# Kernel tuning notes

Hardware: AMD Instinct MI355X
Metric: run time of the kernel (lower is better)

## Reference

```python
import jax, jax.numpy as jnp
import numpy as np

B = 128          # batch size
N_KG = 500       # KG vertices
N = N_KG + 2     # + sensor node + zero target node
D = 1024         # embed_dim (hard-coded in forward)
H = 256          # gnn_hidden
E = 4000         # edges
EPS = 1e-5


def setup_inputs() -> dict:
    key = jax.random.key(0)
    ks = jax.random.split(key, 8)
    return {
        "sensor_batch": jax.random.normal(ks[0], (B, D), jnp.float32),
        "base_vertices": jax.random.normal(ks[1], (N_KG, D), jnp.float32),
        "edge_index": jax.random.randint(ks[2], (2, E), 0, N, jnp.int64),
        "W1": jax.random.normal(ks[3], (D, H), jnp.float32) * (1.0 / np.sqrt(D)),
        "b1": jnp.zeros((H,), jnp.float32),
        "gamma1": jnp.ones((H,), jnp.float32),
        "beta1": jnp.zeros((H,), jnp.float32),
        "W2": jax.random.normal(ks[4], (H, H), jnp.float32) * (1.0 / np.sqrt(H)),
        "b2": jnp.zeros((H,), jnp.float32),
        "gamma2": jnp.ones((H,), jnp.float32),
        "beta2": jnp.zeros((H,), jnp.float32),
        "W3": jax.random.normal(ks[5], (H, H), jnp.float32) * (1.0 / np.sqrt(H)),
        "b3": jnp.zeros((H,), jnp.float32),
        "gamma3": jnp.ones((H,), jnp.float32),
        "beta3": jnp.zeros((H,), jnp.float32),
    }


def _gcn_norm(edge_index):
    # add self loops, symmetric normalization D^{-1/2} A D^{-1/2}
    loops = jnp.arange(N, dtype=edge_index.dtype)
    src = jnp.concatenate([edge_index[0], loops])
    dst = jnp.concatenate([edge_index[1], loops])
    deg = jnp.zeros((N,), jnp.float32).at[dst].add(1.0)
    dinv = jnp.where(deg > 0, jax.lax.rsqrt(deg), 0.0)
    norm = dinv[src] * dinv[dst]   # [E+N]
    return src, dst, norm


def _gcn_conv(x, W, b, src, dst, norm):
    # x: [B, N, F_in] -> [B, N, F_out]
    h = jnp.einsum('bnf,fh->bnh', x, W)
    msg = h[:, src, :] * norm[None, :, None]            # gather + scale
    out = jnp.zeros_like(h).at[:, dst, :].add(msg)      # scatter-add
    return out + b


def _bn_elu(x, gamma, beta):
    # BatchNorm1d over flattened (B*N, H) in training mode, then ELU
    Bn, Nn, Hh = x.shape
    xf = x.reshape(Bn * Nn, Hh)
    mean = jnp.mean(xf, axis=0)
    var = jnp.mean(jnp.square(xf - mean), axis=0)  # biased, as in torch BN fwd
    y = (xf - mean) * jax.lax.rsqrt(var + EPS) * gamma + beta
    return jax.nn.elu(y).reshape(Bn, Nn, Hh)


def reference(sensor_batch, base_vertices, edge_index,
              W1, b1, gamma1, beta1,
              W2, b2, gamma2, beta2,
              W3, b3, gamma3, beta3):
    Bn = sensor_batch.shape[0]
    # x = [base_vertices; sensor_input; zeros] per batch element -> [B, N, D]
    base = jnp.broadcast_to(base_vertices[None], (Bn, N_KG, D))
    zeros = jnp.zeros((Bn, 1, D), sensor_batch.dtype)
    x = jnp.concatenate([base, sensor_batch[:, None, :], zeros], axis=1)

    src, dst, norm = _gcn_norm(edge_index)
    x = _bn_elu(_gcn_conv(x, W1, b1, src, dst, norm), gamma1, beta1)
    x = _bn_elu(_gcn_conv(x, W2, b2, src, dst, norm), gamma2, beta2)
    x = _bn_elu(_gcn_conv(x, W3, b3, src, dst, norm), gamma3, beta3)
    return x
```

## Files before the change

kernel.cpp:

```cpp
#include <hip/hip_runtime.h>
#include <cstdint>
#include <cstddef>

#define NNODES 502
#define NKG    500
#define NPAD   512
#define NEDGE  4000
#define NET    4502
#define BB     128
#define DD     1024
#define HH     256
#define MROWS  (BB*NNODES)
#define MT     65536
#define MCAT   628
#define EPITCH 136

typedef short short8 __attribute__((ext_vector_type(8)));
typedef float f32x4  __attribute__((ext_vector_type(4)));

__device__ __forceinline__ unsigned short f2bf(float f) {
  union { float f; unsigned int u; } v; v.f = f;
  unsigned int r = v.u + 0x7fffu + ((v.u >> 16) & 1u);
  return (unsigned short)(r >> 16);
}

__device__ __forceinline__ float bf2f(unsigned short u) {
  union { unsigned int u; float f; } v; v.u = ((unsigned int)u) << 16;
  return v.f;
}

__device__ __forceinline__ float elu(float y) {
  return (y > 0.f) ? y : (__expf(y) - 1.f);
}

__device__ __forceinline__ void stage16(const void* g, void* l) {
  __builtin_amdgcn_global_load_lds((__attribute__((address_space(1))) void*)g,
                                   (__attribute__((address_space(3))) void*)l, 16, 0, 0);
}

__device__ __forceinline__ void mfma16(f32x4& c, short8 a, short8 b) {
  asm volatile("v_mfma_f32_16x16x32_bf16 %0, %1, %2, %0" : "+v"(c) : "v"(a), "v"(b));
}

__device__ inline void get_edge(const int* __restrict__ e, int i, int i64mode,
                                int& src, int& dst) {
  if (i < NEDGE) {
    if (i64mode) { src = e[2*i]; dst = e[2*NEDGE + 2*i]; }
    else         { src = e[i];   dst = e[NEDGE + i]; }
  } else {
    src = dst = i - NEDGE;
  }
  src = min(max(src, 0), NNODES-1);
  dst = min(max(dst, 0), NNODES-1);
}

__global__ void detect_kernel(const int* __restrict__ e, int* __restrict__ flag) {
  int v = e[2*threadIdx.x + 1];
  if (v != 0) atomicOr(flag, 1);
}

__global__ void deg_kernel(const int* __restrict__ e, const int* __restrict__ flag,
                           int* __restrict__ deg) {
  int i = blockIdx.x*256 + threadIdx.x;
  if (i >= NET) return;
  int src, dst; get_edge(e, i, *flag == 0, src, dst);
  atomicAdd(&deg[dst], 1);
}

__global__ void scan_kernel(const int* __restrict__ deg, float* __restrict__ dinv,
                            int* __restrict__ rp, int* __restrict__ cursor) {
  __shared__ int s[512];
  int t = threadIdx.x;
  int cnt = (t < NNODES) ? deg[t] : 0;
  s[t] = cnt;
  if (t < NNODES) dinv[t] = rsqrtf((float)cnt);
  __syncthreads();
  for (int off = 1; off < 512; off <<= 1) {
    int v = (t >= off) ? s[t-off] : 0;
    __syncthreads();
    s[t] += v;
    __syncthreads();
  }
  if (t == 0) rp[0] = 0;
  if (t < NNODES) { rp[t+1] = s[t]; cursor[t] = s[t] - cnt; }
}

__global__ void fill_kernel(const int* __restrict__ e, const int* __restrict__ flag,
                            const float* __restrict__ dinv, int* __restrict__ cursor,
                            int* __restrict__ colA, float* __restrict__ valA) {
  int i = blockIdx.x*256 + threadIdx.x;
  if (i >= NET) return;
  int src, dst; get_edge(e, i, *flag == 0, src, dst);
  int pos = atomicAdd(&cursor[dst], 1);
  colA[pos] = src;
  valA[pos] = dinv[src] * dinv[dst];
}

__global__ void sdf_kernel(const int* __restrict__ e, const int* __restrict__ flag,
                           const float* __restrict__ dinv, float* __restrict__ Sdf) {
  int i = blockIdx.x*256 + threadIdx.x;
  if (i >= NET) return;
  int src, dst; get_edge(e, i, *flag == 0, src, dst);
  atomicAdd(&Sdf[dst*NPAD + src], dinv[src]*dinv[dst]);
}

__global__ void sdcvt_kernel(const float* __restrict__ Sdf, unsigned short* __restrict__ Sd) {
  int i = blockIdx.x*256 + threadIdx.x;
  Sd[i] = f2bf(Sdf[i]);
}

__global__ __launch_bounds__(256) void prep_kernel(
    const float* __restrict__ W1, const float* __restrict__ W2, const float* __restrict__ W3,
    const float* __restrict__ base, const float* __restrict__ sensor,
    unsigned short* __restrict__ Wt1, unsigned short* __restrict__ Wt2,
    unsigned short* __restrict__ Wt3, unsigned short* __restrict__ Xp1) {
  int bid = blockIdx.x, tid = threadIdx.x;
  if (bid < 512) {
    const float* W = (bid & 256) ? W3 : W2;
    unsigned short* Wt = (bid & 256) ? Wt3 : Wt2;
    int n = bid & 255;
    Wt[n*HH + tid] = f2bf(W[(size_t)tid*HH + n]);
  } else if (bid < 768) {
    int n = bid - 512;
    for (int k = tid; k < DD; k += 256)
      Wt1[n*DD + k] = f2bf(W1[(size_t)k*HH + n]);
  } else {
    int i = (bid - 768)*256 + tid;
    int r = i >> 8, c = (i & 255) * 4;
    float4 v = make_float4(0.f, 0.f, 0.f, 0.f);
    if (r < NKG) v = *(const float4*)&base[(size_t)r*DD + c];
    else if (r < MCAT) v = *(const float4*)&sensor[(size_t)(r-NKG)*DD + c];
    union { unsigned short u[4]; uint2 d; } p;
    p.u[0]=f2bf(v.x); p.u[1]=f2bf(v.y); p.u[2]=f2bf(v.z); p.u[3]=f2bf(v.w);
    *(uint2*)&Xp1[(size_t)r*DD + c] = p.d;
  }
}

__global__ __launch_bounds__(256) void gemm1m_kernel(
    const unsigned short* __restrict__ Ag,
    const unsigned short* __restrict__ Bg,
    float* __restrict__ C) {
  __shared__ unsigned short As[128*32];
  __shared__ unsigned short Bs[128*32];
  int tid = threadIdx.x;
  int wave = tid >> 6, lane = tid & 63;
  int l15 = lane & 15, quad = lane >> 4;
  int wm = (wave & 1) * 64, wn = (wave >> 1) * 64;
  int row0 = blockIdx.y * 128, col0 = blockIdx.x * 128;
  f32x4 acc[4][4] = {};
  for (int k0 = 0; k0 < DD; k0 += 32) {
#pragma unroll
    for (int q = 0; q < 2; ++q) {
      int c = wave*128 + q*64 + lane;
      stage16(Ag + (size_t)(row0 + (c>>2))*DD + k0 + (c&3)*8, As + c*8);
      stage16(Bg + (size_t)(col0 + (c>>2))*DD + k0 + (c&3)*8, Bs + c*8);
    }
    __syncthreads();
    short8 af[4], bfv[4];
#pragma unroll
    for (int i = 0; i < 4; ++i) {
      af[i]  = *(const short8*)(As + (wm + i*16 + l15)*32 + quad*8);
      bfv[i] = *(const short8*)(Bs + (wn + i*16 + l15)*32 + quad*8);
    }
#pragma unroll
    for (int mi = 0; mi < 4; ++mi)
#pragma unroll
      for (int ni = 0; ni < 4; ++ni)
        mfma16(acc[mi][ni], af[mi], bfv[ni]);
    __syncthreads();
  }
  asm volatile("s_nop 7\n\ts_nop 7" ::);
#pragma unroll
  for (int ni = 0; ni < 4; ++ni) {
    int n = col0 + wn + ni*16 + l15;
#pragma unroll
    for (int mi = 0; mi < 4; ++mi) {
      int m = row0 + wm + mi*16 + quad*4;
#pragma unroll
      for (int r = 0; r < 4; ++r)
        if (m + r < MCAT) C[(size_t)(m+r)*HH + n] = acc[mi][ni][r];
    }
  }
}

__global__ void ac_kernel(const int* __restrict__ rp, const int* __restrict__ colA,
                          const float* __restrict__ valA, const float* __restrict__ hcat,
                          float* __restrict__ Abuf, float* __restrict__ cbuf) {
  int n = blockIdx.x, h = threadIdx.x;
  int s = rp[n], e = rp[n+1];
  float acc = 0.f, cacc = 0.f;
  for (int t = s; t < e; ++t) {
    int cl = colA[t]; float v = valA[t];
    if (cl < NKG) acc += v * hcat[cl*HH + h];
    else if (cl == NKG) cacc += v;
  }
  Abuf[n*HH + h] = acc;
  if (h == 0) cbuf[n] = cacc;
}

__global__ __launch_bounds__(256) void bn1n_kernel(
    const float* __restrict__ Abuf, const float* __restrict__ cbuf,
    const float* __restrict__ hcat,
    float* __restrict__ sA1, float* __restrict__ sAA1, float* __restrict__ sAc1,
    float* __restrict__ scp, float* __restrict__ ssA, float* __restrict__ sssA) {
  int bid = blockIdx.x, h = threadIdx.x;
  if (bid < 32) {
    int n0 = bid*16, n1 = min(n0+16, NNODES);
    float sA = 0, sAA = 0, sAc = 0, sc = 0, scc = 0;
    for (int n = n0; n < n1; ++n) {
      float a = Abuf[n*HH + h]; float cn = cbuf[n];
      sA += a; sAA += a*a; sAc += a*cn; sc += cn; scc += cn*cn;
    }
    atomicAdd(&sA1[h], sA); atomicAdd(&sAA1[h], sAA); atomicAdd(&sAc1[h], sAc);
    if (h == 0) { atomicAdd(&scp[0], sc); atomicAdd(&scp[1], scc); }
  } else {
    int b0 = (bid-32)*16;
    float ss = 0, sss = 0;
    for (int b = b0; b < b0+16; ++b) {
      float v = hcat[(size_t)(NKG + b)*HH + h]; ss += v; sss += v*v;
    }
    atomicAdd(&ssA[h], ss); atomicAdd(&sssA[h], sss);
  }
}

__global__ void fin1_kernel(const float* __restrict__ sA1, const float* __restrict__ sAA1,
                            const float* __restrict__ sAc1, const float* __restrict__ scp,
                            const float* __restrict__ ssA, const float* __restrict__ sssA,
                            const float* __restrict__ gamma, const float* __restrict__ beta,
                            float* __restrict__ scale, float* __restrict__ shift) {
  int h = threadIdx.x;
  float sA = sA1[h], sAA = sAA1[h], sAc = sAc1[h];
  float sc = scp[0], scc = scp[1];
  float ss = ssA[h], sss = sssA[h];
  const float cnt = (float)MROWS;
  float mean = ((float)BB * sA + sc*ss) / cnt;
  float msq  = ((float)BB * sAA + 2.f*sAc*ss + scc*sss) / cnt;
  float var  = msq - mean*mean;
  float scl  = gamma[h] * rsqrtf(var + 1e-5f);
  scale[h] = scl; shift[h] = beta[h] - mean*scl;
}

__global__ __launch_bounds__(256) void x2_kernel(
    const float* __restrict__ Abuf, const float* __restrict__ cbuf,
    const float* __restrict__ hcat, const float* __restrict__ scale,
    const float* __restrict__ shift, unsigned short* __restrict__ Xb) {
  int idx = blockIdx.x*256 + threadIdx.x;
  int row = idx >> 6, h0 = (idx & 63)*4;
  int b = row >> 9, n = row & (NPAD-1);
  union { unsigned short u[4]; uint2 d; } p;
  p.d = make_uint2(0,0);
  if (n < NNODES) {
    float4 a  = *(const float4*)(Abuf + n*HH + h0);
    float4 s  = *(const float4*)(hcat + (size_t)(NKG + b)*HH + h0);
    float4 sc = *(const float4*)(scale + h0);
    float4 sh = *(const float4*)(shift + h0);
    float cn = cbuf[n];
    p.u[0] = f2bf(elu((a.x + cn*s.x)*sc.x + sh.x));
    p.u[1] = f2bf(elu((a.y + cn*s.y)*sc.y + sh.y));
    p.u[2] = f2bf(elu((a.z + cn*s.z)*sc.z + sh.z));
    p.u[3] = f2bf(elu((a.w + cn*s.w)*sc.w + sh.w));
  }
  *(uint2*)(Xb + (size_t)row*HH + h0) = p.d;
}

__global__ __launch_bounds__(256) void gemmT_kernel(
    const unsigned short* __restrict__ Ag,
    const unsigned short* __restrict__ Bg,
    unsigned short* __restrict__ Tt) {
  __shared__ __align__(16) unsigned short smem[128*EPITCH];
  unsigned short* As = smem;
  unsigned short* Bs = smem + 8192;
  int tid = threadIdx.x;
  int wave = tid >> 6, lane = tid & 63;
  int l15 = lane & 15, quad = lane >> 4;
  int wm = (wave & 1) * 64, wn = (wave >> 1) * 64;
  int row0 = blockIdx.y * 128, col0 = blockIdx.x * 128;
  f32x4 acc[4][4] = {};
  for (int k0 = 0; k0 < HH; k0 += 64) {
#pragma unroll
    for (int q = 0; q < 4; ++q) {
      int c = q*256 + wave*64 + lane;
      int half = c >> 9, rr = (c >> 2) & 127, j = c & 3;
      stage16(Ag + (size_t)(row0 + rr)*HH + k0 + half*32 + j*8, As + c*8);
      stage16(Bg + (size_t)(col0 + rr)*HH + k0 + half*32 + j*8, Bs + c*8);
    }
    __syncthreads();
#pragma unroll
    for (int kb = 0; kb < 2; ++kb) {
      short8 af[4], bfv[4];
#pragma unroll
      for (int i = 0; i < 4; ++i) {
        af[i]  = *(const short8*)(As + kb*4096 + (wm + i*16 + l15)*32 + quad*8);
        bfv[i] = *(const short8*)(Bs + kb*4096 + (wn + i*16 + l15)*32 + quad*8);
      }
#pragma unroll
      for (int mi = 0; mi < 4; ++mi)
#pragma unroll
        for (int ni = 0; ni < 4; ++ni)
          mfma16(acc[mi][ni], af[mi], bfv[ni]);
    }
    __syncthreads();
  }
  asm volatile("s_nop 7\n\ts_nop 7" ::);
#pragma unroll
  for (int ni = 0; ni < 4; ++ni) {
    int nl = wn + ni*16 + l15;
#pragma unroll
    for (int mi = 0; mi < 4; ++mi) {
      int ml = wm + mi*16 + quad*4;
#pragma unroll
      for (int r = 0; r < 4; ++r)
        smem[nl*EPITCH + ml + r] = f2bf(acc[mi][ni][r]);
    }
  }
  __syncthreads();
  int moff = (tid & 15)*8;
#pragma unroll
  for (int j = 0; j < 8; ++j) {
    int nr = (tid >> 4) + j*16;
    uint4 d = *(const uint4*)(smem + nr*EPITCH + moff);
    *(uint4*)(Tt + (size_t)(col0 + nr)*MT + row0 + moff) = d;
  }
}

__global__ __launch_bounds__(256) void gemmS_kernel(
    const unsigned short* __restrict__ Sd,
    const unsigned short* __restrict__ Tt,
    unsigned short* __restrict__ Xbo,
    float* __restrict__ sums, float* __restrict__ ssqs) {
  __shared__ __align__(16) unsigned short smem[128*EPITCH];
  unsigned short* As = smem;
  unsigned short* Bs = smem + 8192;
  int tid = threadIdx.x;
  int wave = tid >> 6, lane = tid & 63;
  int l15 = lane & 15, quad = lane >> 4;
  int wm = (wave & 1) * 64, wn = (wave >> 1) * 64;
  int id = blockIdx.x;
  int xcd = id & 7;
  int w = id >> 3;
  int y = w & 3;
  int g = (w >> 2) * 8 + xcd;
  int x = g >> 7;
  int b = g & 127;
  int row0 = y * 128, col0 = x * 128;
  f32x4 acc[4][4] = {};
  for (int k0 = 0; k0 < NPAD; k0 += 64) {
#pragma unroll
    for (int q = 0; q < 4; ++q) {
      int c = q*256 + wave*64 + lane;
      int half = c >> 9, rr = (c >> 2) & 127, j = c & 3;
      stage16(Sd + (size_t)(row0 + rr)*NPAD + k0 + half*32 + j*8, As + c*8);
      stage16(Tt + (size_t)(col0 + rr)*MT + b*NPAD + k0 + half*32 + j*8, Bs + c*8);
    }
    __syncthreads();
#pragma unroll
    for (int kb = 0; kb < 2; ++kb) {
      short8 af[4], bfv[4];
#pragma unroll
      for (int i = 0; i < 4; ++i) {
        af[i]  = *(const short8*)(As + kb*4096 + (wm + i*16 + l15)*32 + quad*8);
        bfv[i] = *(const short8*)(Bs + kb*4096 + (wn + i*16 + l15)*32 + quad*8);
      }
#pragma unroll
      for (int mi = 0; mi < 4; ++mi)
#pragma unroll
        for (int ni = 0; ni < 4; ++ni)
          mfma16(acc[mi][ni], af[mi], bfv[ni]);
    }
    __syncthreads();
  }
  asm volatile("s_nop 7\n\ts_nop 7" ::);
  float ps[4] = {0,0,0,0}, pq[4] = {0,0,0,0};
#pragma unroll
  for (int ni = 0; ni < 4; ++ni)
#pragma unroll
    for (int mi = 0; mi < 4; ++mi)
#pragma unroll
      for (int r = 0; r < 4; ++r) {
        float v = acc[mi][ni][r];
        ps[ni] += v; pq[ni] += v*v;
      }
#pragma unroll
  for (int mi = 0; mi < 4; ++mi) {
    int ml = wm + mi*16 + quad*4;
#pragma unroll
    for (int ni = 0; ni < 4; ++ni) {
      int nl = wn + ni*16 + l15;
#pragma unroll
      for (int r = 0; r < 4; ++r)
        smem[(ml + r)*EPITCH + nl] = f2bf(acc[mi][ni][r]);
    }
  }
  __syncthreads();
  unsigned short* Xrow = Xbo + (size_t)b*NPAD*HH;
  int noff = (tid & 15)*8;
#pragma unroll
  for (int j = 0; j < 8; ++j) {
    int rr = (tid >> 4) + j*16;
    int node = row0 + rr;
    if (node < NNODES) {
      uint4 d = *(const uint4*)(smem + rr*EPITCH + noff);
      *(uint4*)(Xrow + (size_t)node*HH + col0 + noff) = d;
    }
  }
  __syncthreads();
  float* red = (float*)smem;
  red[tid] = 0.f;
  __syncthreads();
#pragma unroll
  for (int ni = 0; ni < 4; ++ni) {
    int cl = wn + ni*16 + l15;
    atomicAdd(&red[cl], ps[ni]);
    atomicAdd(&red[128+cl], pq[ni]);
  }
  __syncthreads();
  if (tid < 128) atomicAdd(&sums[col0+tid], red[tid]);
  else atomicAdd(&ssqs[col0+tid-128], red[tid]);
}

__global__ void finalize_kernel(const float* __restrict__ sums, const float* __restrict__ ssqs,
                                const float* __restrict__ gamma, const float* __restrict__ beta,
                                float* __restrict__ scale, float* __restrict__ shift) {
  int h = threadIdx.x;
  const float cnt = (float)MROWS;
  float mean = sums[h] / cnt;
  float var  = ssqs[h] / cnt - mean*mean;
  float scl  = gamma[h] * rsqrtf(var + 1e-5f);
  scale[h] = scl; shift[h] = beta[h] - mean*scl;
}

__global__ __launch_bounds__(256) void bnip_kernel(
    unsigned short* __restrict__ Xb, const float* __restrict__ scale,
    const float* __restrict__ shift) {
  int idx = blockIdx.x*256 + threadIdx.x;
  int row = idx >> 6, h0 = (idx & 63)*4;
  int n = row & (NPAD-1);
  if (n >= NNODES) return;
  unsigned short* p = Xb + (size_t)row*HH + h0;
  union { unsigned short u[4]; uint2 d; } v;
  v.d = *(uint2*)p;
  float4 sc = *(const float4*)(scale + h0);
  float4 sh = *(const float4*)(shift + h0);
  v.u[0] = f2bf(elu(bf2f(v.u[0])*sc.x + sh.x));
  v.u[1] = f2bf(elu(bf2f(v.u[1])*sc.y + sh.y));
  v.u[2] = f2bf(elu(bf2f(v.u[2])*sc.z + sh.z));
  v.u[3] = f2bf(elu(bf2f(v.u[3])*sc.w + sh.w));
  *(uint2*)p = v.d;
}

__global__ __launch_bounds__(256) void bnout_kernel(
    const unsigned short* __restrict__ Xb, const float* __restrict__ scale,
    const float* __restrict__ shift, float* __restrict__ O) {
  int idx = blockIdx.x*256 + threadIdx.x;
  int row = idx >> 6, h0 = (idx & 63)*4;
  int b = row >> 9, n = row & (NPAD-1);
  if (n >= NNODES) return;
  union { unsigned short u[4]; uint2 d; } v;
  v.d = *(const uint2*)(Xb + (size_t)row*HH + h0);
  float4 sc = *(const float4*)(scale + h0);
  float4 sh = *(const float4*)(shift + h0);
  float4 o;
  o.x = elu(bf2f(v.u[0])*sc.x + sh.x);
  o.y = elu(bf2f(v.u[1])*sc.y + sh.y);
  o.z = elu(bf2f(v.u[2])*sc.z + sh.z);
  o.w = elu(bf2f(v.u[3])*sc.w + sh.w);
  *(float4*)(O + ((size_t)(b*NNODES + n)*HH + h0)) = o;
}

extern "C" void kernel_launch(void* const* d_in, const int* in_sizes, int n_in,
                              void* d_out, int out_size, void* d_ws, size_t ws_size,
                              hipStream_t stream) {
  const float* sensor = (const float*)d_in[0];
  const float* base   = (const float*)d_in[1];
  const int*   eidx   = (const int*)d_in[2];
  const float* W1 = (const float*)d_in[3];
  const float* g1 = (const float*)d_in[5];
  const float* be1= (const float*)d_in[6];
  const float* W2 = (const float*)d_in[7];
  const float* g2 = (const float*)d_in[9];
  const float* be2= (const float*)d_in[10];
  const float* W3 = (const float*)d_in[11];
  const float* g3 = (const float*)d_in[13];
  const float* be3= (const float*)d_in[14];

  char* ws = (char*)d_ws;
  int*   deg    = (int*)(ws + 0);
  float* sum2   = (float*)(ws + 2048);
  float* ssq2   = (float*)(ws + 3072);
  float* sum3   = (float*)(ws + 4096);
  float* ssq3   = (float*)(ws + 5120);
  float* cbuf   = (float*)(ws + 6144);
  int*   cursor = (int*)(ws + 8192);
  int*   flag   = (int*)(ws + 10240);
  float* sA1    = (float*)(ws + 10496);
  float* sAA1   = (float*)(ws + 11520);
  float* sAc1   = (float*)(ws + 12544);
  float* scp    = (float*)(ws + 13568);
  float* ssA    = (float*)(ws + 13824);
  float* sssA   = (float*)(ws + 14848);
  float* dinv   = (float*)(ws + 16384);
  int*   rp     = (int*)(ws + 18432);
  int*   colA   = (int*)(ws + 20480);
  float* valA   = (float*)(ws + 40960);
  float* scale1 = (float*)(ws + 61440);
  float* shift1 = (float*)(ws + 62464);
  float* scale2 = (float*)(ws + 63488);
  float* shift2 = (float*)(ws + 64512);
  float* scale3 = (float*)(ws + 65536);
  float* shift3 = (float*)(ws + 66560);
  float* Abuf   = (float*)(ws + 67584);
  float* hcat   = (float*)(ws + 581632);
  unsigned short* Wt2 = (unsigned short*)(ws + 1224704);
  unsigned short* Wt3 = (unsigned short*)(ws + 1355776);
  unsigned short* Sd  = (unsigned short*)(ws + 1486848);
  unsigned short* Xb  = (unsigned short*)(ws + 2011136);
  unsigned short* Tt  = (unsigned short*)(ws + 35565568UL);
  unsigned short* Xp1 = (unsigned short*)(ws + 35565568UL);
  unsigned short* Wt1 = (unsigned short*)(ws + 35565568UL + 1310720);
  float* out = (float*)d_out;
  float* Sdf = (float*)d_out;

  hipMemsetAsync(ws, 0, 16384, stream);
  hipMemsetAsync(d_out, 0, NPAD*NPAD*4, stream);
  detect_kernel<<<1, 256, 0, stream>>>(eidx, flag);
  deg_kernel<<<(NET+255)/256, 256, 0, stream>>>(eidx, flag, deg);
  scan_kernel<<<1, 512, 0, stream>>>(deg, dinv, rp, cursor);
  fill_kernel<<<(NET+255)/256, 256, 0, stream>>>(eidx, flag, dinv, cursor, colA, valA);
  sdf_kernel<<<(NET+255)/256, 256, 0, stream>>>(eidx, flag, dinv, Sdf);
  sdcvt_kernel<<<(NPAD*NPAD)/256, 256, 0, stream>>>(Sdf, Sd);
  prep_kernel<<<1408, 256, 0, stream>>>(W1, W2, W3, base, sensor, Wt1, Wt2, Wt3, Xp1);

  gemm1m_kernel<<<dim3(2, 5), 256, 0, stream>>>(Xp1, Wt1, hcat);
  ac_kernel<<<NNODES, 256, 0, stream>>>(rp, colA, valA, hcat, Abuf, cbuf);
  bn1n_kernel<<<40, 256, 0, stream>>>(Abuf, cbuf, hcat, sA1, sAA1, sAc1, scp, ssA, sssA);
  fin1_kernel<<<1, 256, 0, stream>>>(sA1, sAA1, sAc1, scp, ssA, sssA, g1, be1, scale1, shift1);
  x2_kernel<<<(MT*64)/256, 256, 0, stream>>>(Abuf, cbuf, hcat, scale1, shift1, Xb);

  gemmT_kernel<<<dim3(2, MT/128), 256, 0, stream>>>(Xb, Wt2, Tt);
  gemmS_kernel<<<1024, 256, 0, stream>>>(Sd, Tt, Xb, sum2, ssq2);
  finalize_kernel<<<1, 256, 0, stream>>>(sum2, ssq2, g2, be2, scale2, shift2);
  bnip_kernel<<<(MT*64)/256, 256, 0, stream>>>(Xb, scale2, shift2);

  gemmT_kernel<<<dim3(2, MT/128), 256, 0, stream>>>(Xb, Wt3, Tt);
  gemmS_kernel<<<1024, 256, 0, stream>>>(Sd, Tt, Xb, sum3, ssq3);
  finalize_kernel<<<1, 256, 0, stream>>>(sum3, ssq3, g3, be3, scale3, shift3);
  bnout_kernel<<<(MT*64)/256, 256, 0, stream>>>(Xb, scale3, shift3, out);
}
```

Measured before the change: 323.7 us.

## Fuse BN2+ELU into layer-3 GEMM prologue, split-K first GEMM, merge graph prep kernels

The layer-2 batch-norm finalize and in-place BN/ELU pass are folded into the prologue of the layer-3 transform GEMM. Each block computes scale and shift from the sums and applies BN+ELU to its A tile while staging it. The transform GEMM now covers all 256 output columns per block, so A is read once instead of twice, at the cost of more accumulator registers. The first GEMM is split four ways along K with atomicAdd into a zeroed output to expose more blocks. Edge-format detection, the fill step and the Sdf scatter are merged into fewer kernels to cut launch overhead.

```diff
diff --git a/kernel.cpp b/kernel.cpp
--- a/kernel.cpp
+++ b/kernel.cpp
@@ -54,16 +54,20 @@
   dst = min(max(dst, 0), NNODES-1);
 }
 
-__global__ void detect_kernel(const int* __restrict__ e, int* __restrict__ flag) {
-  int v = e[2*threadIdx.x + 1];
-  if (v != 0) atomicOr(flag, 1);
-}
-
-__global__ void deg_kernel(const int* __restrict__ e, const int* __restrict__ flag,
-                           int* __restrict__ deg) {
+__device__ __forceinline__ int detect_mode(const int* __restrict__ e) {
+  __shared__ int sflag;
+  if (threadIdx.x == 0) sflag = 0;
+  __syncthreads();
+  if (e[2*threadIdx.x + 1] != 0) atomicOr(&sflag, 1);
+  __syncthreads();
+  return sflag == 0;
+}
+
+__global__ void deg_kernel(const int* __restrict__ e, int* __restrict__ deg) {
+  int i64 = detect_mode(e);
   int i = blockIdx.x*256 + threadIdx.x;
   if (i >= NET) return;
-  int src, dst; get_edge(e, i, *flag == 0, src, dst);
+  int src, dst; get_edge(e, i, i64, src, dst);
   atomicAdd(&deg[dst], 1);
 }
 
@@ -85,23 +89,18 @@
   if (t < NNODES) { rp[t+1] = s[t]; cursor[t] = s[t] - cnt; }
 }
 
-__global__ void fill_kernel(const int* __restrict__ e, const int* __restrict__ flag,
-                            const float* __restrict__ dinv, int* __restrict__ cursor,
-                            int* __restrict__ colA, float* __restrict__ valA) {
+__global__ void fillsdf_kernel(const int* __restrict__ e, const float* __restrict__ dinv,
+                               int* __restrict__ cursor, int* __restrict__ colA,
+                               float* __restrict__ valA, float* __restrict__ Sdf) {
+  int i64 = detect_mode(e);
   int i = blockIdx.x*256 + threadIdx.x;
   if (i >= NET) return;
-  int src, dst; get_edge(e, i, *flag == 0, src, dst);
+  int src, dst; get_edge(e, i, i64, src, dst);
+  float v = dinv[src] * dinv[dst];
   int pos = atomicAdd(&cursor[dst], 1);
   colA[pos] = src;
-  valA[pos] = dinv[src] * dinv[dst];
-}
-
-__global__ void sdf_kernel(const int* __restrict__ e, const int* __restrict__ flag,
-                           const float* __restrict__ dinv, float* __restrict__ Sdf) {
-  int i = blockIdx.x*256 + threadIdx.x;
-  if (i >= NET) return;
-  int src, dst; get_edge(e, i, *flag == 0, src, dst);
-  atomicAdd(&Sdf[dst*NPAD + src], dinv[src]*dinv[dst]);
+  valA[pos] = v;
+  atomicAdd(&Sdf[dst*NPAD + src], v);
 }
 
 __global__ void sdcvt_kernel(const float* __restrict__ Sdf, unsigned short* __restrict__ Sd) {
@@ -113,7 +112,8 @@
     const float* __restrict__ W1, const float* __restrict__ W2, const float* __restrict__ W3,
     const float* __restrict__ base, const float* __restrict__ sensor,
     unsigned short* __restrict__ Wt1, unsigned short* __restrict__ Wt2,
-    unsigned short* __restrict__ Wt3, unsigned short* __restrict__ Xp1) {
+    unsigned short* __restrict__ Wt3, unsigned short* __restrict__ Xp1,
+    float* __restrict__ hcatz) {
   int bid = blockIdx.x, tid = threadIdx.x;
   if (bid < 512) {
     const float* W = (bid & 256) ? W3 : W2;
@@ -124,7 +124,7 @@
     int n = bid - 512;
     for (int k = tid; k < DD; k += 256)
       Wt1[n*DD + k] = f2bf(W1[(size_t)k*HH + n]);
-  } else {
+  } else if (bid < 1408) {
     int i = (bid - 768)*256 + tid;
     int r = i >> 8, c = (i & 255) * 4;
     float4 v = make_float4(0.f, 0.f, 0.f, 0.f);
@@ -133,6 +133,8 @@
     union { unsigned short u[4]; uint2 d; } p;
     p.u[0]=f2bf(v.x); p.u[1]=f2bf(v.y); p.u[2]=f2bf(v.z); p.u[3]=f2bf(v.w);
     *(uint2*)&Xp1[(size_t)r*DD + c] = p.d;
+  } else {
+    hcatz[(bid - 1408)*256 + tid] = 0.f;
   }
 }
 
@@ -147,8 +149,9 @@
   int l15 = lane & 15, quad = lane >> 4;
   int wm = (wave & 1) * 64, wn = (wave >> 1) * 64;
   int row0 = blockIdx.y * 128, col0 = blockIdx.x * 128;
+  int kbase = blockIdx.z * 256;
   f32x4 acc[4][4] = {};
-  for (int k0 = 0; k0 < DD; k0 += 32) {
+  for (int k0 = kbase; k0 < kbase + 256; k0 += 32) {
 #pragma unroll
     for (int q = 0; q < 2; ++q) {
       int c = wave*128 + q*64 + lane;
@@ -178,7 +181,7 @@
       int m = row0 + wm + mi*16 + quad*4;
 #pragma unroll
       for (int r = 0; r < 4; ++r)
-        if (m + r < MCAT) C[(size_t)(m+r)*HH + n] = acc[mi][ni][r];
+        if (m + r < MCAT) atomicAdd(&C[(size_t)(m+r)*HH + n], acc[mi][ni][r]);
     }
   }
 }
@@ -263,63 +266,98 @@
   *(uint2*)(Xb + (size_t)row*HH + h0) = p.d;
 }
 
-__global__ __launch_bounds__(256) void gemmT_kernel(
+template<int FBN>
+__global__ __launch_bounds__(256) void gemmT2_kernel(
     const unsigned short* __restrict__ Ag,
     const unsigned short* __restrict__ Bg,
+    const float* __restrict__ sums, const float* __restrict__ ssqs,
+    const float* __restrict__ gamma, const float* __restrict__ beta,
     unsigned short* __restrict__ Tt) {
-  __shared__ __align__(16) unsigned short smem[128*EPITCH];
+  __shared__ __align__(16) unsigned short smem[25600];
   unsigned short* As = smem;
   unsigned short* Bs = smem + 8192;
+  float* sclL = (float*)(smem + 24576);
+  float* shfL = sclL + 256;
   int tid = threadIdx.x;
   int wave = tid >> 6, lane = tid & 63;
   int l15 = lane & 15, quad = lane >> 4;
-  int wm = (wave & 1) * 64, wn = (wave >> 1) * 64;
-  int row0 = blockIdx.y * 128, col0 = blockIdx.x * 128;
-  f32x4 acc[4][4] = {};
+  int wm = (wave & 1) * 64;
+  int wnh = wave >> 1;
+  int row0 = blockIdx.x * 128;
+  if (FBN) {
+    float mean = sums[tid] * (1.f/(float)MROWS);
+    float var  = ssqs[tid] * (1.f/(float)MROWS) - mean*mean;
+    float s = gamma[tid] * rsqrtf(var + 1e-5f);
+    sclL[tid] = s; shfL[tid] = beta[tid] - mean*s;
+    __syncthreads();
+  }
+  f32x4 acc[4][8] = {};
   for (int k0 = 0; k0 < HH; k0 += 64) {
 #pragma unroll
+    for (int q = 0; q < 8; ++q) {
+      int c = q*256 + tid;
+      int kb = c >> 10, rr = (c >> 2) & 255, j = c & 3;
+      stage16(Bg + (size_t)rr*HH + k0 + kb*32 + j*8, Bs + c*8);
+    }
+#pragma unroll
     for (int q = 0; q < 4; ++q) {
-      int c = q*256 + wave*64 + lane;
+      int c = q*256 + tid;
       int half = c >> 9, rr = (c >> 2) & 127, j = c & 3;
-      stage16(Ag + (size_t)(row0 + rr)*HH + k0 + half*32 + j*8, As + c*8);
-      stage16(Bg + (size_t)(col0 + rr)*HH + k0 + half*32 + j*8, Bs + c*8);
+      int kk = k0 + half*32 + j*8;
+      if (FBN) {
+        union { unsigned short u[8]; uint4 d; } va, pa;
+        va.d = *(const uint4*)(Ag + (size_t)(row0 + rr)*HH + kk);
+#pragma unroll
+        for (int t = 0; t < 8; ++t)
+          pa.u[t] = f2bf(elu(bf2f(va.u[t])*sclL[kk+t] + shfL[kk+t]));
+        *(uint4*)(As + c*8) = pa.d;
+      } else {
+        stage16(Ag + (size_t)(row0 + rr)*HH + kk, As + c*8);
+      }
     }
     __syncthreads();
 #pragma unroll
     for (int kb = 0; kb < 2; ++kb) {
-      short8 af[4], bfv[4];
-#pragma unroll
-      for (int i = 0; i < 4; ++i) {
-        af[i]  = *(const short8*)(As + kb*4096 + (wm + i*16 + l15)*32 + quad*8);
-        bfv[i] = *(const short8*)(Bs + kb*4096 + (wn + i*16 + l15)*32 + quad*8);
+      short8 af[4], bfv[8];
+#pragma unroll
+      for (int i = 0; i < 4; ++i)
+        af[i] = *(const short8*)(As + kb*4096 + (wm + i*16 + l15)*32 + quad*8);
+#pragma unroll
+      for (int i = 0; i < 8; ++i)
+        bfv[i] = *(const short8*)(Bs + kb*8192 + (wnh*128 + i*16 + l15)*32 + quad*8);
+#pragma unroll
+      for (int mi = 0; mi < 4; ++mi)
+#pragma unroll
+        for (int ni = 0; ni < 8; ++ni)
+          mfma16(acc[mi][ni], af[mi], bfv[ni]);
+    }
+    __syncthreads();
+  }
+  asm volatile("s_nop 7\n\ts_nop 7" ::);
+  int moff = (tid & 15)*8;
+#pragma unroll
+  for (int nh = 0; nh < 2; ++nh) {
+    if (wnh == nh) {
+#pragma unroll
+      for (int ni = 0; ni < 8; ++ni) {
+        int nl = ni*16 + l15;
+#pragma unroll
+        for (int mi = 0; mi < 4; ++mi) {
+          int ml = wm + mi*16 + quad*4;
+#pragma unroll
+          for (int r = 0; r < 4; ++r)
+            smem[nl*EPITCH + ml + r] = f2bf(acc[mi][ni][r]);
+        }
       }
-#pragma unroll
-      for (int mi = 0; mi < 4; ++mi)
-#pragma unroll
-        for (int ni = 0; ni < 4; ++ni)
-          mfma16(acc[mi][ni], af[mi], bfv[ni]);
-    }
-    __syncthreads();
-  }
-  asm volatile("s_nop 7\n\ts_nop 7" ::);
-#pragma unroll
-  for (int ni = 0; ni < 4; ++ni) {
-    int nl = wn + ni*16 + l15;
-#pragma unroll
-    for (int mi = 0; mi < 4; ++mi) {
-      int ml = wm + mi*16 + quad*4;
-#pragma unroll
-      for (int r = 0; r < 4; ++r)
-        smem[nl*EPITCH + ml + r] = f2bf(acc[mi][ni][r]);
-    }
-  }
-  __syncthreads();
-  int moff = (tid & 15)*8;
-#pragma unroll
-  for (int j = 0; j < 8; ++j) {
-    int nr = (tid >> 4) + j*16;
-    uint4 d = *(const uint4*)(smem + nr*EPITCH + moff);
-    *(uint4*)(Tt + (size_t)(col0 + nr)*MT + row0 + moff) = d;
+    }
+    __syncthreads();
+#pragma unroll
+    for (int j = 0; j < 8; ++j) {
+      int nr = (tid >> 4) + j*16;
+      uint4 d = *(const uint4*)(smem + nr*EPITCH + moff);
+      *(uint4*)(Tt + (size_t)(nh*128 + nr)*MT + row0 + moff) = d;
+    }
+    __syncthreads();
   }
 }
 
@@ -429,25 +467,6 @@
   scale[h] = scl; shift[h] = beta[h] - mean*scl;
 }
 
-__global__ __launch_bounds__(256) void bnip_kernel(
-    unsigned short* __restrict__ Xb, const float* __restrict__ scale,
-    const float* __restrict__ shift) {
-  int idx = blockIdx.x*256 + threadIdx.x;
-  int row = idx >> 6, h0 = (idx & 63)*4;
-  int n = row & (NPAD-1);
-  if (n >= NNODES) return;
-  unsigned short* p = Xb + (size_t)row*HH + h0;
-  union { unsigned short u[4]; uint2 d; } v;
-  v.d = *(uint2*)p;
-  float4 sc = *(const float4*)(scale + h0);
-  float4 sh = *(const float4*)(shift + h0);
-  v.u[0] = f2bf(elu(bf2f(v.u[0])*sc.x + sh.x));
-  v.u[1] = f2bf(elu(bf2f(v.u[1])*sc.y + sh.y));
-  v.u[2] = f2bf(elu(bf2f(v.u[2])*sc.z + sh.z));
-  v.u[3] = f2bf(elu(bf2f(v.u[3])*sc.w + sh.w));
-  *(uint2*)p = v.d;
-}
-
 __global__ __launch_bounds__(256) void bnout_kernel(
     const unsigned short* __restrict__ Xb, const float* __restrict__ scale,
     const float* __restrict__ shift, float* __restrict__ O) {
@@ -491,7 +510,6 @@
   float* ssq3   = (float*)(ws + 5120);
   float* cbuf   = (float*)(ws + 6144);
   int*   cursor = (int*)(ws + 8192);
-  int*   flag   = (int*)(ws + 10240);
   float* sA1    = (float*)(ws + 10496);
   float* sAA1   = (float*)(ws + 11520);
   float* sAc1   = (float*)(ws + 12544);
@@ -504,8 +522,6 @@
   float* valA   = (float*)(ws + 40960);
   float* scale1 = (float*)(ws + 61440);
   float* shift1 = (float*)(ws + 62464);
-  float* scale2 = (float*)(ws + 63488);
-  float* shift2 = (float*)(ws + 64512);
   float* scale3 = (float*)(ws + 65536);
   float* shift3 = (float*)(ws + 66560);
   float* Abuf   = (float*)(ws + 67584);
@@ -522,26 +538,21 @@
 
   hipMemsetAsync(ws, 0, 16384, stream);
   hipMemsetAsync(d_out, 0, NPAD*NPAD*4, stream);
-  detect_kernel<<<1, 256, 0, stream>>>(eidx, flag);
-  deg_kernel<<<(NET+255)/256, 256, 0, stream>>>(eidx, flag, deg);
+  deg_kernel<<<(NET+255)/256, 256, 0, stream>>>(eidx, deg);
   scan_kernel<<<1, 512, 0, stream>>>(deg, dinv, rp, cursor);
-  fill_kernel<<<(NET+255)/256, 256, 0, stream>>>(eidx, flag, dinv, cursor, colA, valA);
-  sdf_kernel<<<(NET+255)/256, 256, 0, stream>>>(eidx, flag, dinv, Sdf);
+  fillsdf_kernel<<<(NET+255)/256, 256, 0, stream>>>(eidx, dinv, cursor, colA, valA, Sdf);
   sdcvt_kernel<<<(NPAD*NPAD)/256, 256, 0, stream>>>(Sdf, Sd);
-  prep_kernel<<<1408, 256, 0, stream>>>(W1, W2, W3, base, sensor, Wt1, Wt2, Wt3, Xp1);
-
-  gemm1m_kernel<<<dim3(2, 5), 256, 0, stream>>>(Xp1, Wt1, hcat);
+  prep_kernel<<<2036, 256, 0, stream>>>(W1, W2, W3, base, sensor, Wt1, Wt2, Wt3, Xp1, hcat);
+
+  gemm1m_kernel<<<dim3(2, 5, 4), 256, 0, stream>>>(Xp1, Wt1, hcat);
   ac_kernel<<<NNODES, 256, 0, stream>>>(rp, colA, valA, hcat, Abuf, cbuf);
   bn1n_kernel<<<40, 256, 0, stream>>>(Abuf, cbuf, hcat, sA1, sAA1, sAc1, scp, ssA, sssA);
   fin1_kernel<<<1, 256, 0, stream>>>(sA1, sAA1, sAc1, scp, ssA, sssA, g1, be1, scale1, shift1);
   x2_kernel<<<(MT*64)/256, 256, 0, stream>>>(Abuf, cbuf, hcat, scale1, shift1, Xb);
 
-  gemmT_kernel<<<dim3(2, MT/128), 256, 0, stream>>>(Xb, Wt2, Tt);
+  gemmT2_kernel<0><<<MT/128, 256, 0, stream>>>(Xb, Wt2, sum2, ssq2, g2, be2, Tt);
   gemmS_kernel<<<1024, 256, 0, stream>>>(Sd, Tt, Xb, sum2, ssq2);
-  finalize_kernel<<<1, 256, 0, stream>>>(sum2, ssq2, g2, be2, scale2, shift2);
-  bnip_kernel<<<(MT*64)/256, 256, 0, stream>>>(Xb, scale2, shift2);
-
-  gemmT_kernel<<<dim3(2, MT/128), 256, 0, stream>>>(Xb, Wt3, Tt);
+  gemmT2_kernel<1><<<MT/128, 256, 0, stream>>>(Xb, Wt3, sum2, ssq2, g2, be2, Tt);
   gemmS_kernel<<<1024, 256, 0, stream>>>(Sd, Tt, Xb, sum3, ssq3);
   finalize_kernel<<<1, 256, 0, stream>>>(sum3, ssq3, g3, be3, scale3, shift3);
   bnout_kernel<<<(MT*64)/256, 256, 0, stream>>>(Xb, scale3, shift3, out);
```

After: 314.1 us. -2.9%, faster.
